# Kernel optimization log

Measured on AMD Instinct MI355X. Metric: run time of the kernel, lower is better.

Reference implementation:

```python
import jax, jax.numpy as jnp
import numpy as np
from jax import lax


def setup_inputs() -> dict:
    key = jax.random.key(0)
    k1, k2 = jax.random.split(key)
    B, C, H, W = 4, 64, 64, 64
    foreground = jax.random.normal(k1, (B, C, H, W), dtype=jnp.float32)
    masks = jax.random.uniform(k2, (B, 1, H, W), dtype=jnp.float32)
    return {"foreground": foreground, "masks": masks}


def reference(foreground, masks):
    # First-call path of KnowledgeConsistentAttention (att_scores_prev is None).
    # patch_size=3 -> padding=1 around 1x1 dynamic kernels; propagate_size=3 -> 3x3 sum pool.
    B, C, H, W = foreground.shape
    P = H * W
    # Dynamic 1x1 kernels: one per spatial location, L2-normalized over channels.
    K = foreground.reshape(B, C, P).transpose(0, 2, 1)            # [B, P, C]
    norm = jnp.sqrt(jnp.sum(K * K, axis=2, keepdims=True))        # flatten(1).norm per kernel
    K = K / (norm + 1e-8)
    # conv2d with 1x1 kernels and padding=1 == GEMM over zero-padded input.
    Xpad = jnp.pad(foreground, ((0, 0), (0, 0), (1, 1), (1, 1)))  # [B, C, H+2, W+2]
    scores = jnp.einsum('bpc,bchw->bphw', K, Xpad)                # [B, P, H+2, W+2]
    # avg_pool2d(k=3, stride=1, pad=1) * 9 == zero-padded 3x3 sum pool.
    scores = lax.reduce_window(scores, jnp.float32(0.0), lax.add,
                               (1, 1, 3, 3), (1, 1, 1, 1), 'SAME')
    attn = jax.nn.softmax(scores, axis=1)                          # softmax over P kernels
    # conv_transpose2d with 1x1 kernels, padding=1 crops the border back to HxW.
    out = jnp.einsum('bphw,bpc->bchw', attn[:, :, 1:-1, 1:-1], K)  # [B, C, H, W]
    return out
```

## Files before the change

kernel.cpp:

```cpp
#include <hip/hip_runtime.h>
#include <hip/hip_bf16.h>
#include <math.h>

#define Bn 4
#define Cn 64
#define Pn 4096
#define QT 32
#define PBK 128
#define NITER (Pn / PBK)
#define LOG2E 1.4426950408889634f

typedef __attribute__((ext_vector_type(8))) short short8;
typedef __attribute__((ext_vector_type(4))) float float4v;
typedef unsigned short bfu;

__device__ __forceinline__ bfu f2bf(float x) {
    unsigned u = __float_as_uint(x);
    u = (u + 0x7fffu + ((u >> 16) & 1u)) >> 16;
    return (bfu)u;
}

__device__ __forceinline__ void async_load16(const bfu* g, bfu* l) {
    __builtin_amdgcn_global_load_lds(
        (const __attribute__((address_space(1))) unsigned int*)(const void*)g,
        (__attribute__((address_space(3))) unsigned int*)(void*)l,
        16, 0, 0);
}

__global__ __launch_bounds__(256) void prep_kernel(const float* __restrict__ fg,
                                                   bfu* __restrict__ Kpc,
                                                   bfu* __restrict__ Kcp,
                                                   float* __restrict__ S) {
    __shared__ float shbuf[64 * 64];
    int t = threadIdx.x;
    if (blockIdx.x < 512) {
        float* tile  = shbuf;
        float* rnorm = shbuf + 64 * 33;
        int b  = blockIdx.x >> 7;
        int p0 = (blockIdx.x & 127) << 5;
        const float* src = fg + (size_t)b * Cn * Pn + p0;
        #pragma unroll
        for (int i = 0; i < 8; ++i) {
            int idx = i * 256 + t;
            int c = idx >> 5, p = idx & 31;
            tile[c * 33 + p] = src[(size_t)c * Pn + p];
        }
        __syncthreads();
        if (t < 32) {
            float ss = 0.f;
            #pragma unroll
            for (int c = 0; c < 64; ++c) { float v = tile[c * 33 + t]; ss += v * v; }
            rnorm[t] = 1.0f / (sqrtf(ss) + 1e-8f);
        }
        __syncthreads();
        bfu* dpc = Kpc + ((size_t)b * Pn + p0) * Cn;
        #pragma unroll
        for (int i = 0; i < 8; ++i) {
            int idx = i * 256 + t;
            int p = idx >> 6, c = idx & 63;
            dpc[(size_t)p * Cn + c] = f2bf(tile[c * 33 + p] * rnorm[p]);
        }
        bfu* dcp = Kcp + (size_t)b * Cn * Pn + p0;
        #pragma unroll
        for (int i = 0; i < 8; ++i) {
            int idx = i * 256 + t;
            int c = idx >> 5, p = idx & 31;
            dcp[(size_t)c * Pn + p] = f2bf(tile[c * 33 + p] * rnorm[p]);
        }
    } else {
        float (*pl)[64] = (float(*)[64])shbuf;
        int bc = blockIdx.x - 512;
        const float* src = fg + (size_t)bc * Pn;
        float*       dst = S  + (size_t)bc * Pn;
        #pragma unroll
        for (int i = 0; i < 16; ++i) {
            int idx = i * 256 + t;
            pl[idx >> 6][idx & 63] = src[idx];
        }
        __syncthreads();
        #pragma unroll
        for (int i = 0; i < 16; ++i) {
            int idx = i * 256 + t;
            int h = idx >> 6, w = idx & 63;
            float s = 0.f;
            #pragma unroll
            for (int dh = -1; dh <= 1; ++dh) {
                int hh = h + dh;
                if (hh < 0 || hh >= 64) continue;
                #pragma unroll
                for (int dw = -1; dw <= 1; ++dw) {
                    int ww = w + dw;
                    if (ww < 0 || ww >= 64) continue;
                    s += pl[hh][ww];
                }
            }
            dst[idx] = s * LOG2E;
        }
    }
}

__global__ __launch_bounds__(512, 2) void flash_kernel(const bfu* __restrict__ Kpc,
                                                       const bfu* __restrict__ Kcp,
                                                       const float* __restrict__ S,
                                                       float* __restrict__ out) {
    __shared__ __align__(16) bfu smem[2 * PBK * 64 + 2 * Cn * PBK + QT * 64 + QT * PBK];
    __shared__ float wredl[8][QT];
    bfu* Sl = smem + 2 * PBK * 64 + 2 * Cn * PBK;
    bfu* El = Sl + QT * 64;

    int b  = blockIdx.x >> 7;
    int q0 = (blockIdx.x & 127) * QT;
    int t  = threadIdx.x;
    int w = t >> 6, l = t & 63, lq = l & 15, quad = l >> 4;

    const float* Sg  = S   + (size_t)b * Cn * Pn;
    const bfu*   gpc = Kpc + (size_t)b * Pn * Cn;
    const bfu*   gcp = Kcp + (size_t)b * Cn * Pn;

    {
        int c = t >> 3, qq = (t & 7) * 4;
        const float* sp = &Sg[(size_t)c * Pn + q0 + qq];
        float4 v0 = *(const float4*)sp;
        float vv[4] = {v0.x, v0.y, v0.z, v0.w};
        int ch = c >> 3, cl = c & 7;
        #pragma unroll
        for (int i = 0; i < 4; ++i) {
            int row = qq + i;
            Sl[row * 64 + ((ch ^ (row & 7)) << 3) + cl] = f2bf(vv[i]);
        }
    }

    #pragma unroll
    for (int j = 0; j < 2; ++j) {
        int g = j * 8 + w;
        int ci = g * 64 + l;
        int row = ci >> 3, chp = ci & 7;
        async_load16(gpc + (size_t)row * Cn + ((chp ^ (row & 7)) << 3), smem + g * 512);
    }
    #pragma unroll
    for (int j = 0; j < 2; ++j) {
        int g = j * 8 + w;
        int ci = g * 64 + l;
        int c = ci >> 4, chp = ci & 15;
        async_load16(gcp + (size_t)c * Pn + ((chp ^ (c & 15)) << 3),
                     smem + 2 * PBK * 64 + g * 512);
    }
    __syncthreads();

    short8 bs[2][2];
    #pragma unroll
    for (int nt = 0; nt < 2; ++nt)
        #pragma unroll
        for (int ks = 0; ks < 2; ++ks) {
            int row = nt * 16 + lq;
            bs[nt][ks] = *(const short8*)&Sl[row * 64 + (((ks * 4 + quad) ^ (lq & 7)) << 3)];
        }

    float4v o[2];
    o[0] = (float4v){0.f, 0.f, 0.f, 0.f};
    o[1] = (float4v){0.f, 0.f, 0.f, 0.f};
    float lacc[2] = {0.f, 0.f};

    int h  = w >> 2;
    int ca = (w & 3) * 16;

    for (int pb = 0; pb < NITER; ++pb) {
        bfu* KpcC = smem + (pb & 1) * (PBK * 64);
        bfu* KcpC = smem + 2 * PBK * 64 + (pb & 1) * (Cn * PBK);

        if (pb + 1 < NITER) {
            bfu* KpcN = smem + ((pb + 1) & 1) * (PBK * 64);
            bfu* KcpN = smem + 2 * PBK * 64 + ((pb + 1) & 1) * (Cn * PBK);
            const bfu* gpc_n = gpc + (size_t)(pb + 1) * PBK * Cn;
            const bfu* gcp_n = gcp + (size_t)(pb + 1) * PBK;
            #pragma unroll
            for (int j = 0; j < 2; ++j) {
                int g = j * 8 + w;
                int ci = g * 64 + l;
                int row = ci >> 3, chp = ci & 7;
                async_load16(gpc_n + (size_t)row * Cn + ((chp ^ (row & 7)) << 3),
                             KpcN + g * 512);
            }
            #pragma unroll
            for (int j = 0; j < 2; ++j) {
                int g = j * 8 + w;
                int ci = g * 64 + l;
                int c = ci >> 4, chp = ci & 15;
                async_load16(gcp_n + (size_t)c * Pn + ((chp ^ (c & 15)) << 3),
                             KcpN + g * 512);
            }
        }

        short8 af[2];
        #pragma unroll
        for (int ks = 0; ks < 2; ++ks) {
            int row = w * 16 + lq;
            af[ks] = *(const short8*)&KpcC[row * 64 + (((ks * 4 + quad) ^ (lq & 7)) << 3)];
        }
        float4v sc[2];
        #pragma unroll
        for (int nt = 0; nt < 2; ++nt) {
            float4v acc = (float4v){0.f, 0.f, 0.f, 0.f};
            acc = __builtin_amdgcn_mfma_f32_16x16x32_bf16(af[0], bs[nt][0], acc, 0, 0, 0);
            acc = __builtin_amdgcn_mfma_f32_16x16x32_bf16(af[1], bs[nt][1], acc, 0, 0, 0);
            sc[nt] = acc;
        }

        #pragma unroll
        for (int nt = 0; nt < 2; ++nt) {
            int row = nt * 16 + lq;
            float e0 = __builtin_amdgcn_exp2f(sc[nt][0]);
            float e1 = __builtin_amdgcn_exp2f(sc[nt][1]);
            float e2 = __builtin_amdgcn_exp2f(sc[nt][2]);
            float e3 = __builtin_amdgcn_exp2f(sc[nt][3]);
            lacc[nt] += (e0 + e1) + (e2 + e3);
            __hip_bfloat162 h01 = __float22bfloat162_rn(make_float2(e0, e1));
            __hip_bfloat162 h23 = __float22bfloat162_rn(make_float2(e2, e3));
            uint2 pk = make_uint2(*(unsigned*)&h01, *(unsigned*)&h23);
            int col = w * 16 + quad * 4;
            int ch = (col >> 3) ^ (row & 15), cl = col & 7;
            *(uint2*)&El[row * PBK + ch * 8 + cl] = pk;
        }
        __syncthreads();

        #pragma unroll
        for (int ks = 0; ks < 2; ++ks) {
            int rowA = ca + lq;
            short8 ak = *(const short8*)&KcpC[rowA * PBK + (((8 * h + ks * 4 + quad) ^ (rowA & 15)) << 3)];
            #pragma unroll
            for (int nt = 0; nt < 2; ++nt) {
                int rowB = nt * 16 + lq;
                short8 bk = *(const short8*)&El[rowB * PBK + (((8 * h + ks * 4 + quad) ^ (rowB & 15)) << 3)];
                o[nt] = __builtin_amdgcn_mfma_f32_16x16x32_bf16(ak, bk, o[nt], 0, 0, 0);
            }
        }
        __syncthreads();
    }

    #pragma unroll
    for (int nt = 0; nt < 2; ++nt) {
        lacc[nt] += __shfl_xor(lacc[nt], 16);
        lacc[nt] += __shfl_xor(lacc[nt], 32);
    }
    if (quad == 0) { wredl[w][lq] = lacc[0]; wredl[w][16 + lq] = lacc[1]; }

    float* Ol = (float*)smem;
    __syncthreads();
    #pragma unroll
    for (int nt = 0; nt < 2; ++nt)
        #pragma unroll
        for (int r = 0; r < 4; ++r)
            Ol[(h * 64 + ca + quad * 4 + r) * 33 + nt * 16 + lq] = o[nt][r];
    __syncthreads();
    float* og = out + (size_t)b * Cn * Pn;
    #pragma unroll
    for (int i = 0; i < 4; ++i) {
        int idx = i * 512 + t;
        int c = idx >> 5, q = idx & 31;
        float lsum = ((wredl[0][q] + wredl[1][q]) + (wredl[2][q] + wredl[3][q])) +
                     ((wredl[4][q] + wredl[5][q]) + (wredl[6][q] + wredl[7][q]));
        float v = (Ol[c * 33 + q] + Ol[(64 + c) * 33 + q]) / lsum;
        og[(size_t)c * Pn + q0 + q] = v;
    }
}

extern "C" void kernel_launch(void* const* d_in, const int* in_sizes, int n_in,
                              void* d_out, int out_size, void* d_ws, size_t ws_size,
                              hipStream_t stream) {
    const float* fg = (const float*)d_in[0];
    float* out = (float*)d_out;
    bfu*   Kpc = (bfu*)d_ws;
    bfu*   Kcp = Kpc + (size_t)Bn * Pn * Cn;
    float* S   = (float*)(Kcp + (size_t)Bn * Pn * Cn);

    prep_kernel <<<768, 256, 0, stream>>>(fg, Kpc, Kcp, S);
    flash_kernel<<<Bn * 128, 512, 0, stream>>>(Kpc, Kcp, S, out);
}
```

Baseline: 102.9 us.

## Load Kcp fragments from global into registers and double-buffer E tile

The Kcp tile is no longer staged through LDS. Each wave now loads its A-fragments for the second GEMM straight from global memory into registers, and the K-split is remapped so every wave covers 32 P-columns and 32 channels. The E tile is double-buffered, so one of the two per-iteration barriers goes away, and Kpc prefetch now runs two stages ahead. Dropping the Kcp buffer cuts LDS use, which lets the launch bound rise to 4 blocks per CU, at the cost of global-latency exposure on the direct loads and a four-way partial-sum reduction in the epilogue.

```diff
diff --git a/kernel.cpp b/kernel.cpp
--- a/kernel.cpp
+++ b/kernel.cpp
@@ -99,19 +99,20 @@
     }
 }
 
-__global__ __launch_bounds__(512, 2) void flash_kernel(const bfu* __restrict__ Kpc,
+__global__ __launch_bounds__(512, 4) void flash_kernel(const bfu* __restrict__ Kpc,
                                                        const bfu* __restrict__ Kcp,
                                                        const float* __restrict__ S,
                                                        float* __restrict__ out) {
-    __shared__ __align__(16) bfu smem[2 * PBK * 64 + 2 * Cn * PBK + QT * 64 + QT * PBK];
+    __shared__ __align__(16) bfu smem[26624];
     __shared__ float wredl[8][QT];
-    bfu* Sl = smem + 2 * PBK * 64 + 2 * Cn * PBK;
-    bfu* El = Sl + QT * 64;
+    bfu* Sl = smem + 16384;
 
     int b  = blockIdx.x >> 7;
     int q0 = (blockIdx.x & 127) * QT;
     int t  = threadIdx.x;
     int w = t >> 6, l = t & 63, lq = l & 15, quad = l >> 4;
+    int cw = w & 1;
+    int kq = w >> 1;
 
     const float* Sg  = S   + (size_t)b * Cn * Pn;
     const bfu*   gpc = Kpc + (size_t)b * Pn * Cn;
@@ -131,19 +132,16 @@
     }
 
     #pragma unroll
-    for (int j = 0; j < 2; ++j) {
-        int g = j * 8 + w;
-        int ci = g * 64 + l;
-        int row = ci >> 3, chp = ci & 7;
-        async_load16(gpc + (size_t)row * Cn + ((chp ^ (row & 7)) << 3), smem + g * 512);
-    }
-    #pragma unroll
-    for (int j = 0; j < 2; ++j) {
-        int g = j * 8 + w;
-        int ci = g * 64 + l;
-        int c = ci >> 4, chp = ci & 15;
-        async_load16(gcp + (size_t)c * Pn + ((chp ^ (c & 15)) << 3),
-                     smem + 2 * PBK * 64 + g * 512);
+    for (int pb0 = 0; pb0 < 2; ++pb0) {
+        const bfu* gsrc = gpc + (size_t)pb0 * PBK * Cn;
+        #pragma unroll
+        for (int j = 0; j < 2; ++j) {
+            int g = j * 8 + w;
+            int ci = g * 64 + l;
+            int row = ci >> 3, chp = ci & 7;
+            async_load16(gsrc + (size_t)row * Cn + ((chp ^ (row & 7)) << 3),
+                         smem + pb0 * 8192 + g * 512);
+        }
     }
     __syncthreads();
 
@@ -156,40 +154,22 @@
             bs[nt][ks] = *(const short8*)&Sl[row * 64 + (((ks * 4 + quad) ^ (lq & 7)) << 3)];
         }
 
-    float4v o[2];
-    o[0] = (float4v){0.f, 0.f, 0.f, 0.f};
-    o[1] = (float4v){0.f, 0.f, 0.f, 0.f};
+    float4v o[2][2];
+    #pragma unroll
+    for (int ct = 0; ct < 2; ++ct)
+        #pragma unroll
+        for (int nt = 0; nt < 2; ++nt) o[ct][nt] = (float4v){0.f, 0.f, 0.f, 0.f};
     float lacc[2] = {0.f, 0.f};
 
-    int h  = w >> 2;
-    int ca = (w & 3) * 16;
-
     for (int pb = 0; pb < NITER; ++pb) {
-        bfu* KpcC = smem + (pb & 1) * (PBK * 64);
-        bfu* KcpC = smem + 2 * PBK * 64 + (pb & 1) * (Cn * PBK);
-
-        if (pb + 1 < NITER) {
-            bfu* KpcN = smem + ((pb + 1) & 1) * (PBK * 64);
-            bfu* KcpN = smem + 2 * PBK * 64 + ((pb + 1) & 1) * (Cn * PBK);
-            const bfu* gpc_n = gpc + (size_t)(pb + 1) * PBK * Cn;
-            const bfu* gcp_n = gcp + (size_t)(pb + 1) * PBK;
-            #pragma unroll
-            for (int j = 0; j < 2; ++j) {
-                int g = j * 8 + w;
-                int ci = g * 64 + l;
-                int row = ci >> 3, chp = ci & 7;
-                async_load16(gpc_n + (size_t)row * Cn + ((chp ^ (row & 7)) << 3),
-                             KpcN + g * 512);
-            }
-            #pragma unroll
-            for (int j = 0; j < 2; ++j) {
-                int g = j * 8 + w;
-                int ci = g * 64 + l;
-                int c = ci >> 4, chp = ci & 15;
-                async_load16(gcp_n + (size_t)c * Pn + ((chp ^ (c & 15)) << 3),
-                             KcpN + g * 512);
-            }
-        }
+        bfu* KpcC = smem + (pb & 1) * 8192;
+        bfu* ElC  = smem + 18432 + (pb & 1) * 4096;
+
+        float4 akr[2];
+        #pragma unroll
+        for (int ct = 0; ct < 2; ++ct)
+            akr[ct] = *(const float4*)&gcp[(size_t)(32 * cw + 16 * ct + lq) * Pn +
+                                           pb * PBK + 32 * kq + quad * 8];
 
         short8 af[2];
         #pragma unroll
@@ -219,22 +199,33 @@
             uint2 pk = make_uint2(*(unsigned*)&h01, *(unsigned*)&h23);
             int col = w * 16 + quad * 4;
             int ch = (col >> 3) ^ (row & 15), cl = col & 7;
-            *(uint2*)&El[row * PBK + ch * 8 + cl] = pk;
-        }
-        __syncthreads();
-
-        #pragma unroll
-        for (int ks = 0; ks < 2; ++ks) {
-            int rowA = ca + lq;
-            short8 ak = *(const short8*)&KcpC[rowA * PBK + (((8 * h + ks * 4 + quad) ^ (rowA & 15)) << 3)];
+            *(uint2*)&ElC[row * PBK + ch * 8 + cl] = pk;
+        }
+
+        __syncthreads();
+
+        if (pb + 2 < NITER) {
+            const bfu* gsrc = gpc + (size_t)(pb + 2) * PBK * Cn;
+            #pragma unroll
+            for (int j = 0; j < 2; ++j) {
+                int g = j * 8 + w;
+                int ci = g * 64 + l;
+                int row = ci >> 3, chp = ci & 7;
+                async_load16(gsrc + (size_t)row * Cn + ((chp ^ (row & 7)) << 3),
+                             KpcC + g * 512);
+            }
+        }
+
+        #pragma unroll
+        for (int ct = 0; ct < 2; ++ct) {
+            short8 ak = *(short8*)&akr[ct];
             #pragma unroll
             for (int nt = 0; nt < 2; ++nt) {
                 int rowB = nt * 16 + lq;
-                short8 bk = *(const short8*)&El[rowB * PBK + (((8 * h + ks * 4 + quad) ^ (rowB & 15)) << 3)];
-                o[nt] = __builtin_amdgcn_mfma_f32_16x16x32_bf16(ak, bk, o[nt], 0, 0, 0);
+                short8 bk = *(const short8*)&ElC[rowB * PBK + (((4 * kq + quad) ^ (rowB & 15)) << 3)];
+                o[ct][nt] = __builtin_amdgcn_mfma_f32_16x16x32_bf16(ak, bk, o[ct][nt], 0, 0, 0);
             }
         }
-        __syncthreads();
     }
 
     #pragma unroll
@@ -247,10 +238,12 @@
     float* Ol = (float*)smem;
     __syncthreads();
     #pragma unroll
-    for (int nt = 0; nt < 2; ++nt)
-        #pragma unroll
-        for (int r = 0; r < 4; ++r)
-            Ol[(h * 64 + ca + quad * 4 + r) * 33 + nt * 16 + lq] = o[nt][r];
+    for (int ct = 0; ct < 2; ++ct)
+        #pragma unroll
+        for (int nt = 0; nt < 2; ++nt)
+            #pragma unroll
+            for (int r = 0; r < 4; ++r)
+                Ol[(kq * 64 + cw * 32 + ct * 16 + quad * 4 + r) * 33 + nt * 16 + lq] = o[ct][nt][r];
     __syncthreads();
     float* og = out + (size_t)b * Cn * Pn;
     #pragma unroll
@@ -259,7 +252,8 @@
         int c = idx >> 5, q = idx & 31;
         float lsum = ((wredl[0][q] + wredl[1][q]) + (wredl[2][q] + wredl[3][q])) +
                      ((wredl[4][q] + wredl[5][q]) + (wredl[6][q] + wredl[7][q]));
-        float v = (Ol[c * 33 + q] + Ol[(64 + c) * 33 + q]) / lsum;
+        float v = ((Ol[c * 33 + q] + Ol[(64 + c) * 33 + q]) +
+                   (Ol[(128 + c) * 33 + q] + Ol[(192 + c) * 33 + q])) / lsum;
         og[(size_t)c * Pn + q0 + q] = v;
     }
 }
```

Result: slower. 107.1 us (+4.0%).
